# Kernel tuning notes

Measured on AMD Instinct MI355X. Metric: run time of the kernel, lower is better.

The kernel has to match this reference:

```python
import jax, jax.numpy as jnp
import numpy as np
import math

B, S, N_UNITS, D_K = 8, 2048, 1024, 512


def setup_inputs() -> dict:
    key = jax.random.key(0)
    ks = jax.random.split(key, 8)
    scale = 1.0 / math.sqrt(N_UNITS)
    query = jax.random.normal(ks[0], (B, S, N_UNITS), dtype=jnp.float32)
    k_in = jax.random.normal(ks[1], (B, S, N_UNITS), dtype=jnp.float32)
    v_in = jax.random.normal(ks[2], (B, S, N_UNITS), dtype=jnp.float32)
    # custom multiplicative mask: causal lower-triangular, broadcast over batch
    mask = jnp.broadcast_to(jnp.tril(jnp.ones((S, S), dtype=jnp.float32)), (B, S, S))
    Wq = jax.random.normal(ks[3], (N_UNITS, D_K), dtype=jnp.float32) * scale
    Wk = jax.random.normal(ks[4], (N_UNITS, D_K), dtype=jnp.float32) * scale
    Wv = jax.random.normal(ks[5], (N_UNITS, D_K), dtype=jnp.float32) * scale
    bq = jnp.zeros((D_K,), dtype=jnp.float32)
    bk = jnp.zeros((D_K,), dtype=jnp.float32)
    bv = jnp.zeros((D_K,), dtype=jnp.float32)
    return {"query": query, "key": k_in, "value": v_in, "mask": mask,
            "Wq": Wq, "bq": bq, "Wk": Wk, "bk": bk, "Wv": Wv, "bv": bv}


def reference(query, key, value, mask, Wq, bq, Wk, bk, Wv, bv):
    d_k = Wq.shape[-1]
    Q = jnp.einsum('bsn,nd->bsd', query, Wq) + bq  # [B,S,Dk]
    K = jnp.einsum('bsn,nd->bsd', key, Wk) + bk
    V = jnp.einsum('bsn,nd->bsd', value, Wv) + bv
    # scores [B,S,S]
    x_hat = jnp.einsum('bqd,bkd->bqk', Q, K) / jnp.sqrt(jnp.float32(d_k))
    # custom multiplicative mask: x*mask - 1e9*(1-mask)
    x_hat_masked = x_hat * mask - 1e9 * (1.0 - mask)
    attn = jax.nn.softmax(x_hat_masked, axis=-1)
    # dropout = 0.0 (eval mode) -> identity
    out = jnp.einsum('bqk,bkd->bqd', attn, V)
    return out
```

## Files before the change

kernel.cpp:

```cpp
#include <hip/hip_runtime.h>

typedef __bf16 bf16_t;
typedef __attribute__((ext_vector_type(4))) __bf16 bf16x4;
typedef __attribute__((ext_vector_type(8))) __bf16 bf16x8;
typedef __attribute__((ext_vector_type(4))) float f32x4;

#define B_    8
#define S_    2048
#define NU    1024
#define DK    512
#define MROWS (B_ * S_)
#define PBATCH (128 * 128 * 136)

#define WAITVM(N) asm volatile("s_waitcnt vmcnt(" #N ")" ::: "memory")
#define WAITLG    asm volatile("s_waitcnt lgkmcnt(0)" ::: "memory")
#define BAR       __builtin_amdgcn_s_barrier()

__device__ __forceinline__ f32x4 mfma16(bf16x8 a, bf16x8 b, f32x4 c) {
  return __builtin_amdgcn_mfma_f32_16x16x32_bf16(a, b, c, 0, 0, 0);
}

__device__ __forceinline__ void async_load16(const void* g, void* l) {
  __builtin_amdgcn_global_load_lds(
      (const __attribute__((address_space(1))) unsigned int*)g,
      (__attribute__((address_space(3))) unsigned int*)l, 16, 0, 0);
}

__device__ __forceinline__ bf16x8 cvt8(f32x4 x0, f32x4 x1) {
  bf16x8 r;
#pragma unroll
  for (int j = 0; j < 4; ++j) { r[j] = (bf16_t)x0[j]; r[j + 4] = (bf16_t)x1[j]; }
  return r;
}

__device__ __forceinline__ void stage_tile(const bf16_t* __restrict__ src,
                                           int rstride, bf16_t* dst, int k0,
                                           int tid) {
#pragma unroll
  for (int j = 0; j < 2; ++j) {
    const int g = j * 256 + tid;
    const int ln = g >> 3, c = g & 7;
    const int cs = c ^ (ln & 7);
    const int srow = 2 * ln + (cs >> 2);
    async_load16(src + (size_t)srow * rstride + k0 + (cs & 3) * 8, dst + g * 8);
  }
}

__device__ __forceinline__ bf16x8 frag(const bf16_t* buf, int row, int q) {
  const int ln = row >> 1;
  const int cp = (((row & 1) << 2) | q) ^ (ln & 7);
  return *(const bf16x8*)(buf + ln * 64 + cp * 8);
}

__global__ __launch_bounds__(256) void transpose_w_kernel(
    const float* __restrict__ Wq, const float* __restrict__ Wk,
    const float* __restrict__ Wv, bf16_t* __restrict__ Wt) {
  const float* W = (blockIdx.z == 0) ? Wq : (blockIdx.z == 1) ? Wk : Wv;
  bf16_t* Wo = Wt + (size_t)blockIdx.z * DK * NU;
  __shared__ float tile[32][33];
  const int t = threadIdx.x;
  const int r = t >> 5, c = t & 31;
  const int kbase = blockIdx.y * 32, nbase = blockIdx.x * 32;
#pragma unroll
  for (int i = 0; i < 4; ++i)
    tile[r + i * 8][c] = W[(size_t)(kbase + r + i * 8) * DK + nbase + c];
  __syncthreads();
#pragma unroll
  for (int i = 0; i < 4; ++i)
    Wo[(size_t)(nbase + r + i * 8) * NU + kbase + c] = (bf16_t)tile[c][r + i * 8];
}

__global__ __launch_bounds__(256) void cvt_kernel(const float* __restrict__ src,
                                                  bf16_t* __restrict__ dst) {
  const size_t t0 = (size_t)blockIdx.x * 256 + threadIdx.x;
#pragma unroll
  for (int it = 0; it < 8; ++it) {
    const size_t i = t0 + (size_t)it * 262144;
    const f32x4 x0 = ((const f32x4*)src)[2 * i];
    const f32x4 x1 = ((const f32x4*)src)[2 * i + 1];
    ((bf16x8*)dst)[i] = cvt8(x0, x1);
  }
}

__global__ __launch_bounds__(256, 3) void xw_gemm_kernel(
    const bf16_t* __restrict__ Xz, const bf16_t* __restrict__ Wz,
    const float* __restrict__ bias, bf16_t* __restrict__ Out, const int vmode) {
  const int bx = blockIdx.x;
  const int m0 = (bx & 127) * 128;
  const int n0 = (bx >> 7) * 128;
  const int tid = threadIdx.x;
  const int wave = tid >> 6, lane = tid & 63;
  const int l16 = lane & 15, quad = lane >> 4;
  const int wm = (wave >> 1) * 64, wn = (wave & 1) * 64;

  __shared__ __align__(16) unsigned char smem[49152];
  bf16_t* a0 = (bf16_t*)smem;
  bf16_t* a1 = (bf16_t*)(smem + 8192);
  bf16_t* a2 = (bf16_t*)(smem + 16384);
  bf16_t* b0 = (bf16_t*)(smem + 24576);
  bf16_t* b1 = (bf16_t*)(smem + 32768);
  bf16_t* b2 = (bf16_t*)(smem + 40960);

  const bf16_t* Ag = Xz + (size_t)m0 * NU;
  const bf16_t* Bg = Wz + (size_t)n0 * NU;

  f32x4 acc[4][4] = {};

#define XW_STAGE(Ad, Bd, K0) \
  { stage_tile(Ag, NU, Ad, K0, tid); stage_tile(Bg, NU, Bd, K0, tid); }
#define XW_COMP(Ac, Bc)                                                       \
  { bf16x8 af[4], bfr[4];                                                     \
    _Pragma("unroll") for (int i = 0; i < 4; ++i)                             \
      af[i] = frag(Ac, wm + i * 16 + l16, quad);                              \
    _Pragma("unroll") for (int j = 0; j < 4; ++j)                             \
      bfr[j] = frag(Bc, wn + j * 16 + l16, quad);                             \
    _Pragma("unroll") for (int i = 0; i < 4; ++i)                             \
      _Pragma("unroll") for (int j = 0; j < 4; ++j)                           \
        acc[i][j] = mfma16(af[i], bfr[j], acc[i][j]); }

  XW_STAGE(a0, b0, 0)
  XW_STAGE(a1, b1, 32)
  const int NS = 32;
  for (int ks = 0; ks < NS; ++ks) {
    if (ks + 1 < NS) { WAITVM(4); } else { WAITVM(0); }
    BAR;
    if (ks + 2 < NS) XW_STAGE(a2, b2, (ks + 2) * 32)
    XW_COMP(a0, b0)
    WAITLG; BAR;
    bf16_t* t = a0; a0 = a1; a1 = a2; a2 = t;
    t = b0; b0 = b1; b1 = b2; b2 = t;
  }

  if (vmode == 0) {
#pragma unroll
    for (int j = 0; j < 4; ++j) {
      const int cn = n0 + wn + j * 16 + l16;
      const float bz = bias[cn];
#pragma unroll
      for (int i = 0; i < 4; ++i) {
        const int rm = m0 + wm + i * 16 + quad * 4;
#pragma unroll
        for (int r = 0; r < 4; ++r)
          Out[(size_t)(rm + r) * DK + cn] = (bf16_t)(acc[i][j][r] + bz);
      }
    }
  } else {
    bf16_t* Ts = (bf16_t*)smem;
#pragma unroll
    for (int j = 0; j < 4; ++j) {
      const int cnl = wn + j * 16 + l16;
      const float bz = bias[n0 + cnl];
#pragma unroll
      for (int i = 0; i < 4; ++i) {
        const int rs = wm + i * 16 + quad * 4;
        bf16x4 t;
#pragma unroll
        for (int r = 0; r < 4; ++r) t[r] = (bf16_t)(acc[i][j][r] + bz);
        *(bf16x4*)&Ts[cnl * 136 + rs] = t;
      }
    }
    WAITLG; BAR;
    const int bb = m0 >> 11, sl = m0 & 2047;
    const int row = tid >> 1, half = tid & 1;
    bf16_t* dst = Out + ((size_t)bb * DK + n0 + row) * S_ + sl + half * 64;
    const bf16_t* sp = &Ts[row * 136 + half * 64];
#pragma unroll
    for (int k = 0; k < 8; ++k)
      *(bf16x8*)(dst + k * 8) = *(const bf16x8*)(sp + k * 8);
  }
#undef XW_STAGE
#undef XW_COMP
}

__global__ __launch_bounds__(256) void zerol_kernel(float* __restrict__ L) {
  ((f32x4*)L)[blockIdx.x * 256 + threadIdx.x] = f32x4{0.f, 0.f, 0.f, 0.f};
}

__global__ __launch_bounds__(256, 3) void qk_p_kernel(
    const bf16_t* __restrict__ Q, const bf16_t* __restrict__ K,
    bf16_t* __restrict__ P, float* __restrict__ L) {
  const int bx = blockIdx.x;
  const int b = bx & 7;
  const int t = bx >> 3;
  int mt = 0;
  while (((mt + 1) * (mt + 2)) / 2 <= t) ++mt;
  const int nt = t - (mt * (mt + 1)) / 2;
  const int klen = (mt + 1) * 128;

  const int tid = threadIdx.x;
  const int wave = tid >> 6, lane = tid & 63;
  const int l16 = lane & 15, quad = lane >> 4;
  const int wm = (wave >> 1) * 64, wn = (wave & 1) * 64;

  __shared__ __align__(16) unsigned char smem[49152];
  bf16_t* a0 = (bf16_t*)smem;
  bf16_t* a1 = (bf16_t*)(smem + 8192);
  bf16_t* a2 = (bf16_t*)(smem + 16384);
  bf16_t* b0 = (bf16_t*)(smem + 24576);
  bf16_t* b1 = (bf16_t*)(smem + 32768);
  bf16_t* b2 = (bf16_t*)(smem + 40960);

  const bf16_t* Ag = Q + (size_t)(b * S_ + mt * 128) * DK;
  const bf16_t* Bg = K + (size_t)(b * S_ + nt * 128) * DK;

  f32x4 acc[4][4] = {};

#define P1_STAGE(Ad, Bd, K0) \
  { stage_tile(Ag, DK, Ad, K0, tid); stage_tile(Bg, DK, Bd, K0, tid); }
#define P1_COMP(Ac, Bc)                                                       \
  { bf16x8 af[4], bfr[4];                                                     \
    _Pragma("unroll") for (int i = 0; i < 4; ++i)                             \
      af[i] = frag(Ac, wm + i * 16 + l16, quad);                              \
    _Pragma("unroll") for (int j = 0; j < 4; ++j)                             \
      bfr[j] = frag(Bc, wn + j * 16 + l16, quad);                             \
    _Pragma("unroll") for (int i = 0; i < 4; ++i)                             \
      _Pragma("unroll") for (int j = 0; j < 4; ++j)                           \
        acc[i][j] = mfma16(af[i], bfr[j], acc[i][j]); }

  P1_STAGE(a0, b0, 0)
  P1_STAGE(a1, b1, 32)
  const int NS = 16;
  for (int ks = 0; ks < NS; ++ks) {
    if (ks + 1 < NS) { WAITVM(4); } else { WAITVM(0); }
    BAR;
    if (ks + 2 < NS) P1_STAGE(a2, b2, (ks + 2) * 32)
    P1_COMP(a0, b0)
    WAITLG; BAR;
    bf16_t* tp = a0; a0 = a1; a1 = a2; a2 = tp;
    tp = b0; b0 = b1; b1 = b2; b2 = tp;
  }

  const float scale = 0.04419417382415922f;
  bf16_t* Pt = P + (size_t)b * PBATCH + (size_t)8192 * mt * (mt + 1);
  float* Lb = L + b * S_ + mt * 128;
#pragma unroll
  for (int i = 0; i < 4; ++i) {
#pragma unroll
    for (int r = 0; r < 4; ++r) {
      const int lrow = wm + i * 16 + quad * 4 + r;
      const int srow = mt * 128 + lrow;
      float rsum = 0.f;
#pragma unroll
      for (int j = 0; j < 4; ++j) {
        const int scol = nt * 128 + wn + j * 16 + l16;
        const float p =
            (scol > srow) ? 0.f : __expf(acc[i][j][r] * scale - 10.0f);
        rsum += p;
        Pt[(size_t)lrow * klen + scol] = (bf16_t)p;
      }
#pragma unroll
      for (int off = 8; off >= 1; off >>= 1)
        rsum += __shfl_xor(rsum, off, 64);
      if (l16 == 0) atomicAdd(&Lb[lrow], rsum);
    }
  }
#undef P1_STAGE
#undef P1_COMP
}

__global__ __launch_bounds__(256, 3) void pv_kernel(
    const bf16_t* __restrict__ P, const bf16_t* __restrict__ Vt,
    const float* __restrict__ L, float* __restrict__ Out) {
  const int bx = blockIdx.x;
  const int b = bx & 7;
  const int u = bx >> 3;
  const int mt = 15 - (u >> 2);
  const int d0 = (u & 3) * 128;
  const int klen = (mt + 1) * 128;
  const int NS = (mt + 1) * 4;

  const int tid = threadIdx.x;
  const int wave = tid >> 6, lane = tid & 63;
  const int l16 = lane & 15, quad = lane >> 4;
  const int wm = (wave >> 1) * 64, wn = (wave & 1) * 64;

  __shared__ __align__(16) unsigned char smem[49152];
  bf16_t* a0 = (bf16_t*)smem;
  bf16_t* a1 = (bf16_t*)(smem + 8192);
  bf16_t* a2 = (bf16_t*)(smem + 16384);
  bf16_t* b0 = (bf16_t*)(smem + 24576);
  bf16_t* b1 = (bf16_t*)(smem + 32768);
  bf16_t* b2 = (bf16_t*)(smem + 40960);

  const bf16_t* Ag = P + (size_t)b * PBATCH + (size_t)8192 * mt * (mt + 1);
  const bf16_t* Bg = Vt + ((size_t)b * DK + d0) * S_;

  f32x4 acc[4][4] = {};

#define P2_STAGE(Ad, Bd, K0) \
  { stage_tile(Ag, klen, Ad, K0, tid); stage_tile(Bg, S_, Bd, K0, tid); }
#define P2_COMP(Ac, Bc)                                                       \
  { bf16x8 af[4], bfr[4];                                                     \
    _Pragma("unroll") for (int i = 0; i < 4; ++i)                             \
      af[i] = frag(Ac, wm + i * 16 + l16, quad);                              \
    _Pragma("unroll") for (int j = 0; j < 4; ++j)                             \
      bfr[j] = frag(Bc, wn + j * 16 + l16, quad);                             \
    _Pragma("unroll") for (int i = 0; i < 4; ++i)                             \
      _Pragma("unroll") for (int j = 0; j < 4; ++j)                           \
        acc[i][j] = mfma16(af[i], bfr[j], acc[i][j]); }

  P2_STAGE(a0, b0, 0)
  P2_STAGE(a1, b1, 32)
  for (int ks = 0; ks < NS; ++ks) {
    if (ks + 1 < NS) { WAITVM(4); } else { WAITVM(0); }
    BAR;
    if (ks + 2 < NS) P2_STAGE(a2, b2, (ks + 2) * 32)
    P2_COMP(a0, b0)
    WAITLG; BAR;
    bf16_t* tp = a0; a0 = a1; a1 = a2; a2 = tp;
    tp = b0; b0 = b1; b1 = b2; b2 = tp;
  }

  const int m0 = b * S_ + mt * 128;
#pragma unroll
  for (int i = 0; i < 4; ++i) {
#pragma unroll
    for (int r = 0; r < 4; ++r) {
      const int grow = m0 + wm + i * 16 + quad * 4 + r;
      const float inv = 1.0f / L[grow];
      float* orow = Out + (size_t)grow * DK + d0;
#pragma unroll
      for (int j = 0; j < 4; ++j)
        orow[wn + j * 16 + l16] = acc[i][j][r] * inv;
    }
  }
#undef P2_STAGE
#undef P2_COMP
}

extern "C" void kernel_launch(void* const* d_in, const int* in_sizes, int n_in,
                              void* d_out, int out_size, void* d_ws, size_t ws_size,
                              hipStream_t stream) {
  const float* query = (const float*)d_in[0];
  const float* key_i = (const float*)d_in[1];
  const float* value = (const float*)d_in[2];
  const float* Wq = (const float*)d_in[4];
  const float* bq = (const float*)d_in[5];
  const float* Wk = (const float*)d_in[6];
  const float* bk = (const float*)d_in[7];
  const float* Wv = (const float*)d_in[8];
  const float* bv = (const float*)d_in[9];
  float* out = (float*)d_out;

  bf16_t* Wt = (bf16_t*)d_ws;
  bf16_t* Qw = Wt + (size_t)3 * DK * NU;
  bf16_t* Kw = Qw + (size_t)MROWS * DK;
  bf16_t* Vw = Kw + (size_t)MROWS * DK;
  bf16_t* Pw = Vw + (size_t)MROWS * DK;
  bf16_t* Xz = Pw;
  float* Lw = (float*)(Pw + (size_t)B_ * PBATCH);

  transpose_w_kernel<<<dim3(16, 32, 3), 256, 0, stream>>>(Wq, Wk, Wv, Wt);
  zerol_kernel<<<16, 256, 0, stream>>>(Lw);

  cvt_kernel<<<1024, 256, 0, stream>>>(query, Xz);
  xw_gemm_kernel<<<512, 256, 0, stream>>>(Xz, Wt, bq, Qw, 0);
  cvt_kernel<<<1024, 256, 0, stream>>>(key_i, Xz);
  xw_gemm_kernel<<<512, 256, 0, stream>>>(Xz, Wt + (size_t)DK * NU, bk, Kw, 0);
  cvt_kernel<<<1024, 256, 0, stream>>>(value, Xz);
  xw_gemm_kernel<<<512, 256, 0, stream>>>(Xz, Wt + (size_t)2 * DK * NU, bv, Vw, 1);

  qk_p_kernel<<<1088, 256, 0, stream>>>(Qw, Kw, Pw, Lw);
  pv_kernel<<<512, 256, 0, stream>>>(Pw, Vw, Lw, out);
}
```

Measured before the change: 458.9 us.

## Batch QKV projections into single launches and drop per-step second barrier

```diff
diff --git a/kernel.cpp b/kernel.cpp
--- a/kernel.cpp
+++ b/kernel.cpp
@@ -14,7 +14,7 @@
 
 #define WAITVM(N) asm volatile("s_waitcnt vmcnt(" #N ")" ::: "memory")
 #define WAITLG    asm volatile("s_waitcnt lgkmcnt(0)" ::: "memory")
-#define BAR       __builtin_amdgcn_s_barrier()
+#define BAR       asm volatile("s_barrier" ::: "memory")
 
 __device__ __forceinline__ f32x4 mfma16(bf16x8 a, bf16x8 b, f32x4 c) {
   return __builtin_amdgcn_mfma_f32_16x16x32_bf16(a, b, c, 0, 0, 0);
@@ -70,9 +70,13 @@
     Wo[(size_t)(nbase + r + i * 8) * NU + kbase + c] = (bf16_t)tile[c][r + i * 8];
 }
 
-__global__ __launch_bounds__(256) void cvt_kernel(const float* __restrict__ src,
-                                                  bf16_t* __restrict__ dst) {
-  const size_t t0 = (size_t)blockIdx.x * 256 + threadIdx.x;
+__global__ __launch_bounds__(256) void cvt3_kernel(
+    const float* __restrict__ q_in, const float* __restrict__ k_in,
+    const float* __restrict__ v_in, bf16_t* __restrict__ Xb) {
+  const int z = blockIdx.x >> 10;
+  const float* src = (z == 0) ? q_in : (z == 1) ? k_in : v_in;
+  bf16_t* dst = Xb + (size_t)z * MROWS * NU;
+  const size_t t0 = (size_t)(blockIdx.x & 1023) * 256 + threadIdx.x;
 #pragma unroll
   for (int it = 0; it < 8; ++it) {
     const size_t i = t0 + (size_t)it * 262144;
@@ -82,56 +86,62 @@
   }
 }
 
-__global__ __launch_bounds__(256, 3) void xw_gemm_kernel(
-    const bf16_t* __restrict__ Xz, const bf16_t* __restrict__ Wz,
-    const float* __restrict__ bias, bf16_t* __restrict__ Out, const int vmode) {
+__global__ __launch_bounds__(256, 3) void xw3_gemm_kernel(
+    const bf16_t* __restrict__ Xb, const bf16_t* __restrict__ Wt,
+    const float* __restrict__ bq, const float* __restrict__ bk,
+    const float* __restrict__ bv, bf16_t* __restrict__ Qo,
+    bf16_t* __restrict__ Ko, bf16_t* __restrict__ Vt) {
   const int bx = blockIdx.x;
-  const int m0 = (bx & 127) * 128;
-  const int n0 = (bx >> 7) * 128;
+  const int z = bx >> 9;
+  const int t = bx & 511;
+  const int m0 = (t & 127) * 128;
+  const int n0 = (t >> 7) * 128;
+  const float* bias = (z == 0) ? bq : (z == 1) ? bk : bv;
+
   const int tid = threadIdx.x;
   const int wave = tid >> 6, lane = tid & 63;
   const int l16 = lane & 15, quad = lane >> 4;
   const int wm = (wave >> 1) * 64, wn = (wave & 1) * 64;
 
   __shared__ __align__(16) unsigned char smem[49152];
-  bf16_t* a0 = (bf16_t*)smem;
-  bf16_t* a1 = (bf16_t*)(smem + 8192);
-  bf16_t* a2 = (bf16_t*)(smem + 16384);
-  bf16_t* b0 = (bf16_t*)(smem + 24576);
-  bf16_t* b1 = (bf16_t*)(smem + 32768);
-  bf16_t* b2 = (bf16_t*)(smem + 40960);
-
-  const bf16_t* Ag = Xz + (size_t)m0 * NU;
-  const bf16_t* Bg = Wz + (size_t)n0 * NU;
+  bf16_t* lds = (bf16_t*)smem;
+
+  const bf16_t* Ag = Xb + (size_t)z * MROWS * NU + (size_t)m0 * NU;
+  const bf16_t* Bg = Wt + (size_t)z * DK * NU + (size_t)n0 * NU;
 
   f32x4 acc[4][4] = {};
 
-#define XW_STAGE(Ad, Bd, K0) \
-  { stage_tile(Ag, NU, Ad, K0, tid); stage_tile(Bg, NU, Bd, K0, tid); }
-#define XW_COMP(Ac, Bc)                                                       \
-  { bf16x8 af[4], bfr[4];                                                     \
-    _Pragma("unroll") for (int i = 0; i < 4; ++i)                             \
-      af[i] = frag(Ac, wm + i * 16 + l16, quad);                              \
-    _Pragma("unroll") for (int j = 0; j < 4; ++j)                             \
-      bfr[j] = frag(Bc, wn + j * 16 + l16, quad);                             \
-    _Pragma("unroll") for (int i = 0; i < 4; ++i)                             \
-      _Pragma("unroll") for (int j = 0; j < 4; ++j)                           \
-        acc[i][j] = mfma16(af[i], bfr[j], acc[i][j]); }
-
-  XW_STAGE(a0, b0, 0)
-  XW_STAGE(a1, b1, 32)
+  stage_tile(Ag, NU, lds, 0, tid);
+  stage_tile(Bg, NU, lds + 12288, 0, tid);
+  stage_tile(Ag, NU, lds + 4096, 32, tid);
+  stage_tile(Bg, NU, lds + 16384, 32, tid);
   const int NS = 32;
+  int cur = 0, nxt2 = 2;
   for (int ks = 0; ks < NS; ++ks) {
     if (ks + 1 < NS) { WAITVM(4); } else { WAITVM(0); }
     BAR;
-    if (ks + 2 < NS) XW_STAGE(a2, b2, (ks + 2) * 32)
-    XW_COMP(a0, b0)
-    WAITLG; BAR;
-    bf16_t* t = a0; a0 = a1; a1 = a2; a2 = t;
-    t = b0; b0 = b1; b1 = b2; b2 = t;
-  }
-
-  if (vmode == 0) {
+    if (ks + 2 < NS) {
+      stage_tile(Ag, NU, lds + nxt2 * 4096, (ks + 2) * 32, tid);
+      stage_tile(Bg, NU, lds + 12288 + nxt2 * 4096, (ks + 2) * 32, tid);
+    }
+    const bf16_t* ac = lds + cur * 4096;
+    const bf16_t* bc = lds + 12288 + cur * 4096;
+    bf16x8 af[4], bfr[4];
+#pragma unroll
+    for (int i = 0; i < 4; ++i) af[i] = frag(ac, wm + i * 16 + l16, quad);
+#pragma unroll
+    for (int j = 0; j < 4; ++j) bfr[j] = frag(bc, wn + j * 16 + l16, quad);
+#pragma unroll
+    for (int i = 0; i < 4; ++i)
+#pragma unroll
+      for (int j = 0; j < 4; ++j)
+        acc[i][j] = mfma16(af[i], bfr[j], acc[i][j]);
+    cur = (cur + 1 == 3) ? 0 : cur + 1;
+    nxt2 = (nxt2 + 1 == 3) ? 0 : nxt2 + 1;
+  }
+
+  if (z != 2) {
+    bf16_t* Out = (z == 0) ? Qo : Ko;
 #pragma unroll
     for (int j = 0; j < 4; ++j) {
       const int cn = n0 + wn + j * 16 + l16;
@@ -145,7 +155,8 @@
       }
     }
   } else {
-    bf16_t* Ts = (bf16_t*)smem;
+    bf16_t* Ts = lds;
+    BAR;
 #pragma unroll
     for (int j = 0; j < 4; ++j) {
       const int cnl = wn + j * 16 + l16;
@@ -153,23 +164,21 @@
 #pragma unroll
       for (int i = 0; i < 4; ++i) {
         const int rs = wm + i * 16 + quad * 4;
-        bf16x4 t;
-#pragma unroll
-        for (int r = 0; r < 4; ++r) t[r] = (bf16_t)(acc[i][j][r] + bz);
-        *(bf16x4*)&Ts[cnl * 136 + rs] = t;
+        bf16x4 tv;
+#pragma unroll
+        for (int r = 0; r < 4; ++r) tv[r] = (bf16_t)(acc[i][j][r] + bz);
+        *(bf16x4*)&Ts[cnl * 136 + rs] = tv;
       }
     }
     WAITLG; BAR;
-    const int bb = m0 >> 11, sl = m0 & 2047;
+    const int bb2 = m0 >> 11, sl = m0 & 2047;
     const int row = tid >> 1, half = tid & 1;
-    bf16_t* dst = Out + ((size_t)bb * DK + n0 + row) * S_ + sl + half * 64;
+    bf16_t* dst = Vt + ((size_t)bb2 * DK + n0 + row) * S_ + sl + half * 64;
     const bf16_t* sp = &Ts[row * 136 + half * 64];
 #pragma unroll
     for (int k = 0; k < 8; ++k)
       *(bf16x8*)(dst + k * 8) = *(const bf16x8*)(sp + k * 8);
   }
-#undef XW_STAGE
-#undef XW_COMP
 }
 
 __global__ __launch_bounds__(256) void zerol_kernel(float* __restrict__ L) {
@@ -193,41 +202,40 @@
   const int wm = (wave >> 1) * 64, wn = (wave & 1) * 64;
 
   __shared__ __align__(16) unsigned char smem[49152];
-  bf16_t* a0 = (bf16_t*)smem;
-  bf16_t* a1 = (bf16_t*)(smem + 8192);
-  bf16_t* a2 = (bf16_t*)(smem + 16384);
-  bf16_t* b0 = (bf16_t*)(smem + 24576);
-  bf16_t* b1 = (bf16_t*)(smem + 32768);
-  bf16_t* b2 = (bf16_t*)(smem + 40960);
+  bf16_t* lds = (bf16_t*)smem;
 
   const bf16_t* Ag = Q + (size_t)(b * S_ + mt * 128) * DK;
   const bf16_t* Bg = K + (size_t)(b * S_ + nt * 128) * DK;
 
   f32x4 acc[4][4] = {};
 
-#define P1_STAGE(Ad, Bd, K0) \
-  { stage_tile(Ag, DK, Ad, K0, tid); stage_tile(Bg, DK, Bd, K0, tid); }
-#define P1_COMP(Ac, Bc)                                                       \
-  { bf16x8 af[4], bfr[4];                                                     \
-    _Pragma("unroll") for (int i = 0; i < 4; ++i)                             \
-      af[i] = frag(Ac, wm + i * 16 + l16, quad);                              \
-    _Pragma("unroll") for (int j = 0; j < 4; ++j)                             \
-      bfr[j] = frag(Bc, wn + j * 16 + l16, quad);                             \
-    _Pragma("unroll") for (int i = 0; i < 4; ++i)                             \
-      _Pragma("unroll") for (int j = 0; j < 4; ++j)                           \
-        acc[i][j] = mfma16(af[i], bfr[j], acc[i][j]); }
-
-  P1_STAGE(a0, b0, 0)
-  P1_STAGE(a1, b1, 32)
+  stage_tile(Ag, DK, lds, 0, tid);
+  stage_tile(Bg, DK, lds + 12288, 0, tid);
+  stage_tile(Ag, DK, lds + 4096, 32, tid);
+  stage_tile(Bg, DK, lds + 16384, 32, tid);
   const int NS = 16;
+  int cur = 0, nxt2 = 2;
   for (int ks = 0; ks < NS; ++ks) {
     if (ks + 1 < NS) { WAITVM(4); } else { WAITVM(0); }
     BAR;
-    if (ks + 2 < NS) P1_STAGE(a2, b2, (ks + 2) * 32)
-    P1_COMP(a0, b0)
-    WAITLG; BAR;
-    bf16_t* tp = a0; a0 = a1; a1 = a2; a2 = tp;
-    tp = b0; b0 = b1; b1 = b2; b2 = tp;
+    if (ks + 2 < NS) {
+      stage_tile(Ag, DK, lds + nxt2 * 4096, (ks + 2) * 32, tid);
+      stage_tile(Bg, DK, lds + 12288 + nxt2 * 4096, (ks + 2) * 32, tid);
+    }
+    const bf16_t* ac = lds + cur * 4096;
+    const bf16_t* bc = lds + 12288 + cur * 4096;
+    bf16x8 af[4], bfr[4];
+#pragma unroll
+    for (int i = 0; i < 4; ++i) af[i] = frag(ac, wm + i * 16 + l16, quad);
+#pragma unroll
+    for (int j = 0; j < 4; ++j) bfr[j] = frag(bc, wn + j * 16 + l16, quad);
+#pragma unroll
+    for (int i = 0; i < 4; ++i)
+#pragma unroll
+      for (int j = 0; j < 4; ++j)
+        acc[i][j] = mfma16(af[i], bfr[j], acc[i][j]);
+    cur = (cur + 1 == 3) ? 0 : cur + 1;
+    nxt2 = (nxt2 + 1 == 3) ? 0 : nxt2 + 1;
   }
 
   const float scale = 0.04419417382415922f;
@@ -254,8 +262,6 @@
       if (l16 == 0) atomicAdd(&Lb[lrow], rsum);
     }
   }
-#undef P1_STAGE
-#undef P1_COMP
 }
 
 __global__ __launch_bounds__(256, 3) void pv_kernel(
@@ -275,40 +281,39 @@
   const int wm = (wave >> 1) * 64, wn = (wave & 1) * 64;
 
   __shared__ __align__(16) unsigned char smem[49152];
-  bf16_t* a0 = (bf16_t*)smem;
-  bf16_t* a1 = (bf16_t*)(smem + 8192);
-  bf16_t* a2 = (bf16_t*)(smem + 16384);
-  bf16_t* b0 = (bf16_t*)(smem + 24576);
-  bf16_t* b1 = (bf16_t*)(smem + 32768);
-  bf16_t* b2 = (bf16_t*)(smem + 40960);
+  bf16_t* lds = (bf16_t*)smem;
 
   const bf16_t* Ag = P + (size_t)b * PBATCH + (size_t)8192 * mt * (mt + 1);
   const bf16_t* Bg = Vt + ((size_t)b * DK + d0) * S_;
 
   f32x4 acc[4][4] = {};
 
-#define P2_STAGE(Ad, Bd, K0) \
-  { stage_tile(Ag, klen, Ad, K0, tid); stage_tile(Bg, S_, Bd, K0, tid); }
-#define P2_COMP(Ac, Bc)                                                       \
-  { bf16x8 af[4], bfr[4];                                                     \
-    _Pragma("unroll") for (int i = 0; i < 4; ++i)                             \
-      af[i] = frag(Ac, wm + i * 16 + l16, quad);                              \
-    _Pragma("unroll") for (int j = 0; j < 4; ++j)                             \
-      bfr[j] = frag(Bc, wn + j * 16 + l16, quad);                             \
-    _Pragma("unroll") for (int i = 0; i < 4; ++i)                             \
-      _Pragma("unroll") for (int j = 0; j < 4; ++j)                           \
-        acc[i][j] = mfma16(af[i], bfr[j], acc[i][j]); }
-
-  P2_STAGE(a0, b0, 0)
-  P2_STAGE(a1, b1, 32)
+  stage_tile(Ag, klen, lds, 0, tid);
+  stage_tile(Bg, S_, lds + 12288, 0, tid);
+  stage_tile(Ag, klen, lds + 4096, 32, tid);
+  stage_tile(Bg, S_, lds + 16384, 32, tid);
+  int cur = 0, nxt2 = 2;
   for (int ks = 0; ks < NS; ++ks) {
     if (ks + 1 < NS) { WAITVM(4); } else { WAITVM(0); }
     BAR;
-    if (ks + 2 < NS) P2_STAGE(a2, b2, (ks + 2) * 32)
-    P2_COMP(a0, b0)
-    WAITLG; BAR;
-    bf16_t* tp = a0; a0 = a1; a1 = a2; a2 = tp;
-    tp = b0; b0 = b1; b1 = b2; b2 = tp;
+    if (ks + 2 < NS) {
+      stage_tile(Ag, klen, lds + nxt2 * 4096, (ks + 2) * 32, tid);
+      stage_tile(Bg, S_, lds + 12288 + nxt2 * 4096, (ks + 2) * 32, tid);
+    }
+    const bf16_t* ac = lds + cur * 4096;
+    const bf16_t* bc = lds + 12288 + cur * 4096;
+    bf16x8 af[4], bfr[4];
+#pragma unroll
+    for (int i = 0; i < 4; ++i) af[i] = frag(ac, wm + i * 16 + l16, quad);
+#pragma unroll
+    for (int j = 0; j < 4; ++j) bfr[j] = frag(bc, wn + j * 16 + l16, quad);
+#pragma unroll
+    for (int i = 0; i < 4; ++i)
+#pragma unroll
+      for (int j = 0; j < 4; ++j)
+        acc[i][j] = mfma16(af[i], bfr[j], acc[i][j]);
+    cur = (cur + 1 == 3) ? 0 : cur + 1;
+    nxt2 = (nxt2 + 1 == 3) ? 0 : nxt2 + 1;
   }
 
   const int m0 = b * S_ + mt * 128;
@@ -324,8 +329,6 @@
         orow[wn + j * 16 + l16] = acc[i][j][r] * inv;
     }
   }
-#undef P2_STAGE
-#undef P2_COMP
 }
 
 extern "C" void kernel_launch(void* const* d_in, const int* in_sizes, int n_in,
@@ -346,20 +349,14 @@
   bf16_t* Qw = Wt + (size_t)3 * DK * NU;
   bf16_t* Kw = Qw + (size_t)MROWS * DK;
   bf16_t* Vw = Kw + (size_t)MROWS * DK;
-  bf16_t* Pw = Vw + (size_t)MROWS * DK;
-  bf16_t* Xz = Pw;
-  float* Lw = (float*)(Pw + (size_t)B_ * PBATCH);
+  bf16_t* Xb = Vw + (size_t)MROWS * DK;
+  bf16_t* Pw = Xb;
+  float* Lw = (float*)(Xb + (size_t)3 * MROWS * NU);
 
   transpose_w_kernel<<<dim3(16, 32, 3), 256, 0, stream>>>(Wq, Wk, Wv, Wt);
   zerol_kernel<<<16, 256, 0, stream>>>(Lw);
-
-  cvt_kernel<<<1024, 256, 0, stream>>>(query, Xz);
-  xw_gemm_kernel<<<512, 256, 0, stream>>>(Xz, Wt, bq, Qw, 0);
-  cvt_kernel<<<1024, 256, 0, stream>>>(key_i, Xz);
-  xw_gemm_kernel<<<512, 256, 0, stream>>>(Xz, Wt + (size_t)DK * NU, bk, Kw, 0);
-  cvt_kernel<<<1024, 256, 0, stream>>>(value, Xz);
-  xw_gemm_kernel<<<512, 256, 0, stream>>>(Xz, Wt + (size_t)2 * DK * NU, bv, Vw, 1);
-
+  cvt3_kernel<<<3072, 256, 0, stream>>>(query, key_i, value, Xb);
+  xw3_gemm_kernel<<<1536, 256, 0, stream>>>(Xb, Wt, bq, bk, bv, Qw, Kw, Vw);
   qk_p_kernel<<<1088, 256, 0, stream>>>(Qw, Kw, Pw, Lw);
   pv_kernel<<<512, 256, 0, stream>>>(Pw, Vw, Lw, out);
 }
```

Result: slower. 468.5 us (+2.1%).
